# Kernel tuning notes

Measured on AMD Instinct MI355X. Metric: run time of the kernel, lower is better.

The kernel has to match this reference:

```python
import jax, jax.numpy as jnp
import numpy as np

# Production-scale dims: tokens T = B*S = 1024, d_model = 768, 8 experts, top-2 routing
B, S, D, E, K = 1, 1024, 768, 8, 2
H = 4 * D  # expert hidden dim


def setup_inputs() -> dict:
    key = jax.random.key(0)
    ks = jax.random.split(key, 6)
    s = jnp.float32(0.02)
    return {
        "x": jax.random.normal(ks[0], (B, S, D), jnp.float32),
        "Wr": jax.random.normal(ks[1], (E, D), jnp.float32) * s,      # router Linear (no bias), torch layout [out,in]
        "W1": jax.random.normal(ks[2], (E, H, D), jnp.float32) * s,   # per-expert first Linear
        "b1": jnp.zeros((E, H), jnp.float32),
        "W2": jax.random.normal(ks[3], (E, D, H), jnp.float32) * s,   # per-expert second Linear
        "b2": jnp.zeros((E, D), jnp.float32),
        "sW1": jax.random.normal(ks[4], (H, D), jnp.float32) * s,     # shared expert
        "sb1": jnp.zeros((H,), jnp.float32),
        "sW2": jax.random.normal(ks[5], (D, H), jnp.float32) * s,
        "sb2": jnp.zeros((D,), jnp.float32),
    }


def reference(x, Wr, W1, b1, W2, b2, sW1, sb1, sW2, sb2):
    Bx, Sx, Dx = x.shape
    xf = x.reshape(-1, Dx)                                   # [T, D]
    T = xf.shape[0]

    # Router: top-k logits, others masked to -inf, then softmax.
    # softmax over -inf-masked logits == softmax over the k kept logits scattered back.
    logits = xf @ Wr.T                                       # [T, E]
    topv, idx = jax.lax.top_k(logits, K)                     # [T, K]
    gate_k = jax.nn.softmax(topv, axis=-1)                   # [T, K]
    gates = jnp.zeros((T, logits.shape[-1]), x.dtype).at[
        jnp.arange(T)[:, None], idx
    ].add(gate_k)                                            # [T, E], zero for unrouted experts

    # Expert MLPs (dense over experts; gate is exactly zero for unrouted -> same math
    # as the original masked gather/scatter loop). Dropout is identity in eval mode.
    h = jax.nn.relu(jnp.einsum('td,ehd->teh', xf, W1) + b1)  # [T, E, H]
    y = jnp.einsum('teh,edh->ted', h, W2) + b2               # [T, E, D]
    moe = jnp.einsum('te,ted->td', gates, y)                 # [T, D]

    # Shared expert: original adds 0.1 * shared(x) once per expert that selected the
    # token; every token is selected by exactly K (distinct top-k) experts.
    sh = jax.nn.relu(xf @ sW1.T + sb1) @ sW2.T + sb2         # [T, D]
    out = moe + (0.1 * K) * sh
    return out.reshape(Bx, Sx, Dx)
```

## Files before the change

kernel.cpp:

```cpp
#include <hip/hip_runtime.h>

#define T_TOK 1024
#define Dm 768
#define Hm 3072
#define NE 8
#define NPACK 3072
#define MAXTILES 32

typedef __attribute__((ext_vector_type(8))) short short8;
typedef __attribute__((ext_vector_type(4))) float f32x4;

__device__ __forceinline__ unsigned f2bf(float f) {
  unsigned u = __builtin_bit_cast(unsigned, f);
  u += 0x7fffu + ((u >> 16) & 1u);
  return u >> 16;
}
__device__ __forceinline__ unsigned pk2bf(float a, float b) {
  return f2bf(a) | (f2bf(b) << 16);
}

__global__ __launch_bounds__(256) void router_kernel(
    const float* __restrict__ x, const float* __restrict__ Wr,
    int* __restrict__ counts, int* __restrict__ tlist, float* __restrict__ glist,
    int4* __restrict__ tok2row, float2* __restrict__ tok2g) {
  __shared__ float sWr[NE * Dm];
  for (int i = threadIdx.x; i < NE * Dm; i += 256) sWr[i] = Wr[i];
  __syncthreads();
  const int wave = threadIdx.x >> 6, lane = threadIdx.x & 63;
  const int t = blockIdx.x * 4 + wave;
  float acc[NE];
#pragma unroll
  for (int e = 0; e < NE; e++) acc[e] = 0.f;
  for (int d = lane; d < Dm; d += 64) {
    float xv = x[t * Dm + d];
#pragma unroll
    for (int e = 0; e < NE; e++) acc[e] += xv * sWr[e * Dm + d];
  }
#pragma unroll
  for (int e = 0; e < NE; e++) {
#pragma unroll
    for (int off = 32; off > 0; off >>= 1) acc[e] += __shfl_down(acc[e], off);
  }
  if (lane == 0) {
    int i0 = 0; float v0 = acc[0];
#pragma unroll
    for (int e = 1; e < NE; e++) if (acc[e] > v0) { v0 = acc[e]; i0 = e; }
    int i1 = -1; float v1 = -1e30f;
#pragma unroll
    for (int e = 0; e < NE; e++) if (e != i0 && acc[e] > v1) { v1 = acc[e]; i1 = e; }
    float g0 = 1.f / (1.f + expf(v1 - v0));
    float g1 = 1.f - g0;
    int p0 = atomicAdd(&counts[i0], 1);
    tlist[i0 * T_TOK + p0] = t; glist[i0 * T_TOK + p0] = g0;
    int p1 = atomicAdd(&counts[i1], 1);
    tlist[i1 * T_TOK + p1] = t; glist[i1 * T_TOK + p1] = g1;
    tok2row[t] = make_int4(i0, p0, i1, p1);
    tok2g[t] = float2{g0, g1};
  }
}

template <int MODE>
__global__ __launch_bounds__(512) void moe_gemm(
    const float* __restrict__ x,
    const float* __restrict__ W1, const float* __restrict__ b1,
    const float* __restrict__ sW1, const float* __restrict__ sb1,
    const float* __restrict__ W2, const float* __restrict__ b2,
    const float* __restrict__ sW2, const float* __restrict__ sb2,
    unsigned short* __restrict__ hbuf, float* __restrict__ ybuf, float* __restrict__ outp,
    const int* __restrict__ counts,
    const int* __restrict__ tlist, const float* __restrict__ glist) {
  int ti = blockIdx.y;
  int e = 0, m0 = 0, pbase = 0, Ne = 0;
  bool found = false;
  for (int ee = 0; ee <= NE; ee++) {
    int ne = (ee < NE) ? counts[ee] : T_TOK;
    int nt = (ne + 127) >> 7;
    if (!found) {
      if (ti < nt) { e = ee; Ne = ne; m0 = ti << 7; found = true; }
      else { ti -= nt; pbase += ne; }
    }
  }
  if (!found) return;
  const int n0 = blockIdx.x * 128;

  constexpr int Kfull = (MODE == 0) ? Dm : Hm;
  constexpr int KC    = (MODE == 0) ? Dm : (Hm / 2);
  constexpr int NK    = KC / 64;
  const int kbase = (MODE == 0) ? 0 : (blockIdx.z * KC);

  const float* Bw;
  const float* bias;
  if constexpr (MODE == 0) {
    Bw   = (e < NE) ? W1 + (size_t)e * Hm * Dm : sW1;
    bias = (e < NE) ? b1 + (size_t)e * Hm : sb1;
  } else {
    Bw   = (e < NE) ? W2 + (size_t)e * Dm * Hm : sW2;
    bias = (e < NE) ? b2 + (size_t)e * Dm : sb2;
  }

  __shared__ unsigned short sA[128][72];
  __shared__ unsigned short sB[128][72];

  const int tid = threadIdx.x;
  const int lane = tid & 63;
  const int wid = tid >> 6;
  const int wr = wid >> 2;
  const int wc = wid & 3;

  const float* aPtrF[4];
  const unsigned short* aPtrH[2];
  if constexpr (MODE == 0) {
#pragma unroll
    for (int c = 0; c < 4; c++) {
      int gi = m0 + c * 32 + (tid >> 4);
      int si = gi < Ne ? gi : Ne - 1;
      int tok = (e < NE) ? tlist[e * T_TOK + si] : si;
      aPtrF[c] = x + (size_t)tok * Dm + (tid & 15) * 4;
    }
  } else {
#pragma unroll
    for (int c = 0; c < 2; c++) {
      int prow = pbase + m0 + c * 64 + (tid >> 3);
      if (prow >= NPACK) prow = NPACK - 1;
      aPtrH[c] = hbuf + (size_t)prow * Hm + kbase + (tid & 7) * 8;
    }
  }
  const float* bPtrF[4];
#pragma unroll
  for (int c = 0; c < 4; c++) {
    int nrow = n0 + c * 32 + (tid >> 4);
    bPtrF[c] = Bw + (size_t)nrow * Kfull + kbase + (tid & 15) * 4;
  }

  f32x4 acc[4][2];
#pragma unroll
  for (int m = 0; m < 4; m++)
#pragma unroll
    for (int n = 0; n < 2; n++) acc[m][n] = (f32x4)0.0f;

  const int rF = tid >> 4;
  const int cF = (tid & 15) * 4;
  const int rH = tid >> 3;
  const int cH = (tid & 7) * 8;
  const int frow = lane & 15;
  const int fk = (lane >> 4) * 8;

  float4 aFA[4], bFA[4], aFB[4], bFB[4];
  uint4 aHA[2], aHB[2];

  auto stage_load_A = [&](int ko) {
    if constexpr (MODE == 0) {
#pragma unroll
      for (int c = 0; c < 4; c++) aFA[c] = *(const float4*)(aPtrF[c] + ko);
    } else {
#pragma unroll
      for (int c = 0; c < 2; c++) aHA[c] = *(const uint4*)(aPtrH[c] + ko);
    }
#pragma unroll
    for (int c = 0; c < 4; c++) bFA[c] = *(const float4*)(bPtrF[c] + ko);
  };
  auto stage_load_B = [&](int ko) {
    if constexpr (MODE == 0) {
#pragma unroll
      for (int c = 0; c < 4; c++) aFB[c] = *(const float4*)(aPtrF[c] + ko);
    } else {
#pragma unroll
      for (int c = 0; c < 2; c++) aHB[c] = *(const uint4*)(aPtrH[c] + ko);
    }
#pragma unroll
    for (int c = 0; c < 4; c++) bFB[c] = *(const float4*)(bPtrF[c] + ko);
  };
  auto stage_write_A = [&]() {
    if constexpr (MODE == 0) {
#pragma unroll
      for (int c = 0; c < 4; c++)
        *(uint2*)&sA[c * 32 + rF][cF] =
            make_uint2(pk2bf(aFA[c].x, aFA[c].y), pk2bf(aFA[c].z, aFA[c].w));
    } else {
#pragma unroll
      for (int c = 0; c < 2; c++) *(uint4*)&sA[c * 64 + rH][cH] = aHA[c];
    }
#pragma unroll
    for (int c = 0; c < 4; c++)
      *(uint2*)&sB[c * 32 + rF][cF] =
          make_uint2(pk2bf(bFA[c].x, bFA[c].y), pk2bf(bFA[c].z, bFA[c].w));
  };
  auto stage_write_B = [&]() {
    if constexpr (MODE == 0) {
#pragma unroll
      for (int c = 0; c < 4; c++)
        *(uint2*)&sA[c * 32 + rF][cF] =
            make_uint2(pk2bf(aFB[c].x, aFB[c].y), pk2bf(aFB[c].z, aFB[c].w));
    } else {
#pragma unroll
      for (int c = 0; c < 2; c++) *(uint4*)&sA[c * 64 + rH][cH] = aHB[c];
    }
#pragma unroll
    for (int c = 0; c < 4; c++)
      *(uint2*)&sB[c * 32 + rF][cF] =
          make_uint2(pk2bf(bFB[c].x, bFB[c].y), pk2bf(bFB[c].z, bFB[c].w));
  };
  auto do_mfma = [&]() {
#pragma unroll
    for (int kk = 0; kk < 2; kk++) {
      short8 af[4], bfr[2];
#pragma unroll
      for (int m = 0; m < 4; m++)
        af[m] = *(const short8*)&sA[wr * 64 + m * 16 + frow][kk * 32 + fk];
#pragma unroll
      for (int n = 0; n < 2; n++)
        bfr[n] = *(const short8*)&sB[wc * 32 + n * 16 + frow][kk * 32 + fk];
#pragma unroll
      for (int m = 0; m < 4; m++)
#pragma unroll
        for (int n = 0; n < 2; n++)
          acc[m][n] = __builtin_amdgcn_mfma_f32_16x16x32_bf16(af[m], bfr[n], acc[m][n], 0, 0, 0);
    }
  };

  stage_load_A(0);
  stage_load_B(64);

  for (int ks = 0; ks < NK; ks += 2) {
    stage_write_A();
    __syncthreads();
    if (ks + 2 < NK) stage_load_A((ks + 2) * 64);
    do_mfma();
    __syncthreads();
    stage_write_B();
    __syncthreads();
    if (ks + 3 < NK) stage_load_B((ks + 3) * 64);
    do_mfma();
    __syncthreads();
  }

#pragma unroll
  for (int m = 0; m < 4; m++) {
    int lr = wr * 64 + m * 16 + (lane >> 4) * 4;
#pragma unroll
    for (int n = 0; n < 2; n++) {
      int gc = n0 + wc * 32 + n * 16 + (lane & 15);
      float bv = bias[gc];
#pragma unroll
      for (int j = 0; j < 4; j++) {
        int gi = m0 + lr + j;
        if (gi >= Ne) continue;
        float v = acc[m][n][j];
        if constexpr (MODE == 0) {
          v += bv;
          v = v > 0.f ? v : 0.f;
          hbuf[(size_t)(pbase + gi) * Hm + gc] = (unsigned short)f2bf(v);
        } else if constexpr (MODE == 1) {
          ybuf[(size_t)blockIdx.z * NPACK * Dm + (size_t)(pbase + gi) * Dm + gc] = v;
        } else {
          int t; float g;
          if (e < NE) { t = tlist[e * T_TOK + gi]; g = glist[e * T_TOK + gi]; }
          else        { t = gi; g = 0.2f; }
          float add = g * (v + (kbase == 0 ? bv : 0.f));
          atomicAdd(&outp[(size_t)t * Dm + gc], add);
        }
      }
    }
  }
}

__global__ __launch_bounds__(256) void finalize_kernel(
    const float* __restrict__ ybuf, const int* __restrict__ counts,
    const int4* __restrict__ tok2row, const float2* __restrict__ tok2g,
    const float* __restrict__ b2, const float* __restrict__ sb2,
    float* __restrict__ out) {
  const int t = blockIdx.x;
  int bases[NE];
  int s = 0;
#pragma unroll
  for (int e = 0; e < NE; e++) { bases[e] = s; s += counts[e]; }
  const int4 rr = tok2row[t];
  const float2 gg = tok2g[t];
  const int r0 = bases[rr.x] + rr.y;
  const int r1 = bases[rr.z] + rr.w;
  const int rs = s + t;
  const float* y0 = ybuf;
  const float* y1 = ybuf + (size_t)NPACK * Dm;
  for (int d = threadIdx.x; d < Dm; d += 256) {
    float v0 = y0[(size_t)r0 * Dm + d] + y1[(size_t)r0 * Dm + d] + b2[rr.x * Dm + d];
    float v1 = y0[(size_t)r1 * Dm + d] + y1[(size_t)r1 * Dm + d] + b2[rr.z * Dm + d];
    float vs = y0[(size_t)rs * Dm + d] + y1[(size_t)rs * Dm + d] + sb2[d];
    out[(size_t)t * Dm + d] = gg.x * v0 + gg.y * v1 + 0.2f * vs;
  }
}

extern "C" void kernel_launch(void* const* d_in, const int* in_sizes, int n_in,
                              void* d_out, int out_size, void* d_ws, size_t ws_size,
                              hipStream_t stream) {
  const float* x   = (const float*)d_in[0];
  const float* Wr  = (const float*)d_in[1];
  const float* W1  = (const float*)d_in[2];
  const float* b1  = (const float*)d_in[3];
  const float* W2  = (const float*)d_in[4];
  const float* b2  = (const float*)d_in[5];
  const float* sW1 = (const float*)d_in[6];
  const float* sb1 = (const float*)d_in[7];
  const float* sW2 = (const float*)d_in[8];
  const float* sb2 = (const float*)d_in[9];
  float* out = (float*)d_out;

  char* ws = (char*)d_ws;
  int*    counts  = (int*)(ws + 0);
  int4*   tok2row = (int4*)(ws + 1024);
  float2* tok2g   = (float2*)(ws + 17408);
  int*    tlist   = (int*)(ws + 25600);
  float*  glist   = (float*)(ws + 58368);
  unsigned short* hbuf = (unsigned short*)(ws + 91136);
  float*  ybuf    = (float*)(ws + 18965504);
  const size_t NEED_YBUF = 37839872;

  (void)hipMemsetAsync(counts, 0, 128, stream);

  router_kernel<<<dim3(T_TOK / 4), 256, 0, stream>>>(x, Wr, counts, tlist, glist,
                                                     tok2row, tok2g);

  moe_gemm<0><<<dim3(Hm / 128, MAXTILES, 1), 512, 0, stream>>>(
      x, W1, b1, sW1, sb1, W2, b2, sW2, sb2, hbuf, ybuf, out, counts, tlist, glist);

  if (ws_size >= NEED_YBUF) {
    moe_gemm<1><<<dim3(Dm / 128, MAXTILES, 2), 512, 0, stream>>>(
        x, W1, b1, sW1, sb1, W2, b2, sW2, sb2, hbuf, ybuf, out, counts, tlist, glist);
    finalize_kernel<<<dim3(T_TOK), 256, 0, stream>>>(ybuf, counts, tok2row, tok2g,
                                                     b2, sb2, out);
  } else {
    (void)hipMemsetAsync(out, 0, (size_t)T_TOK * Dm * sizeof(float), stream);
    moe_gemm<2><<<dim3(Dm / 128, MAXTILES, 2), 512, 0, stream>>>(
        x, W1, b1, sW1, sb1, W2, b2, sW2, sb2, hbuf, ybuf, out, counts, tlist, glist);
  }
}
```

Measured before the change: 371.9 us.

## Drop split-K in second GEMM, use 128x96 tiles, bf16 ybuf, fused shared-expert output

The second expert GEMM no longer splits K across two z-slices. It uses a 128x96 tile with a 4x2 wave layout, so each block covers the full K=3072. Expert outputs go to a bf16 ybuf instead of two fp32 partial buffers, and the shared-expert rows write 0.2*(v+bias) straight into the output, which finalize then accumulates into. Launch grids are flattened to 1D with an N-fastest block ordering, meant to improve weight reuse in cache, and the glist and fallback atomic paths are removed. The aim is to cut ybuf traffic and the finalize reads, at the cost of fewer blocks in the second GEMM (longer K loop per block) and bf16 rounding of expert outputs.

After: 356.6 us. -4.1%, faster.

```diff
diff --git a/kernel.cpp b/kernel.cpp
--- a/kernel.cpp
+++ b/kernel.cpp
@@ -18,10 +18,14 @@
 __device__ __forceinline__ unsigned pk2bf(float a, float b) {
   return f2bf(a) | (f2bf(b) << 16);
 }
+__device__ __forceinline__ float bf2f(unsigned short s) {
+  unsigned u = ((unsigned)s) << 16;
+  return __builtin_bit_cast(float, u);
+}
 
 __global__ __launch_bounds__(256) void router_kernel(
     const float* __restrict__ x, const float* __restrict__ Wr,
-    int* __restrict__ counts, int* __restrict__ tlist, float* __restrict__ glist,
+    int* __restrict__ counts, int* __restrict__ tlist,
     int4* __restrict__ tok2row, float2* __restrict__ tok2g) {
   __shared__ float sWr[NE * Dm];
   for (int i = threadIdx.x; i < NE * Dm; i += 256) sWr[i] = Wr[i];
@@ -51,9 +55,9 @@
     float g0 = 1.f / (1.f + expf(v1 - v0));
     float g1 = 1.f - g0;
     int p0 = atomicAdd(&counts[i0], 1);
-    tlist[i0 * T_TOK + p0] = t; glist[i0 * T_TOK + p0] = g0;
+    tlist[i0 * T_TOK + p0] = t;
     int p1 = atomicAdd(&counts[i1], 1);
-    tlist[i1 * T_TOK + p1] = t; glist[i1 * T_TOK + p1] = g1;
+    tlist[i1 * T_TOK + p1] = t;
     tok2row[t] = make_int4(i0, p0, i1, p1);
     tok2g[t] = float2{g0, g1};
   }
@@ -64,12 +68,24 @@
     const float* __restrict__ x,
     const float* __restrict__ W1, const float* __restrict__ b1,
     const float* __restrict__ sW1, const float* __restrict__ sb1,
-    const float* __restrict__ W2, const float* __restrict__ b2,
-    const float* __restrict__ sW2, const float* __restrict__ sb2,
-    unsigned short* __restrict__ hbuf, float* __restrict__ ybuf, float* __restrict__ outp,
-    const int* __restrict__ counts,
-    const int* __restrict__ tlist, const float* __restrict__ glist) {
-  int ti = blockIdx.y;
+    const float* __restrict__ W2, const float* __restrict__ sW2,
+    const float* __restrict__ sb2,
+    unsigned short* __restrict__ hbuf, unsigned short* __restrict__ ybuf,
+    float* __restrict__ outp,
+    const int* __restrict__ counts, const int* __restrict__ tlist) {
+  constexpr int BN    = (MODE == 0) ? 128 : 96;
+  constexpr int Kfull = (MODE == 0) ? Dm : Hm;
+  constexpr int NK    = Kfull / 64;
+  constexpr int M_REP = (MODE == 0) ? 4 : 2;
+  constexpr int N_REP = (MODE == 0) ? 2 : 3;
+  constexpr int NBR   = BN / 32;
+
+  const int b = blockIdx.x;
+  int nIdx, ti;
+  if constexpr (MODE == 0) { nIdx = (b % 8) + 8 * ((b / 8) % 3); ti = b / 24; }
+  else                     { nIdx = b % 8;                        ti = b / 8;  }
+  const int n0 = nIdx * BN;
+
   int e = 0, m0 = 0, pbase = 0, Ne = 0;
   bool found = false;
   for (int ee = 0; ee <= NE; ee++) {
@@ -81,12 +97,6 @@
     }
   }
   if (!found) return;
-  const int n0 = blockIdx.x * 128;
-
-  constexpr int Kfull = (MODE == 0) ? Dm : Hm;
-  constexpr int KC    = (MODE == 0) ? Dm : (Hm / 2);
-  constexpr int NK    = KC / 64;
-  const int kbase = (MODE == 0) ? 0 : (blockIdx.z * KC);
 
   const float* Bw;
   const float* bias;
@@ -95,17 +105,18 @@
     bias = (e < NE) ? b1 + (size_t)e * Hm : sb1;
   } else {
     Bw   = (e < NE) ? W2 + (size_t)e * Dm * Hm : sW2;
-    bias = (e < NE) ? b2 + (size_t)e * Dm : sb2;
+    bias = sb2;
   }
 
   __shared__ unsigned short sA[128][72];
-  __shared__ unsigned short sB[128][72];
+  __shared__ unsigned short sB[BN][72];
 
   const int tid = threadIdx.x;
   const int lane = tid & 63;
   const int wid = tid >> 6;
-  const int wr = wid >> 2;
-  const int wc = wid & 3;
+  int rb, cb;
+  if constexpr (MODE == 0) { rb = (wid >> 2) * 64; cb = (wid & 3) * 32; }
+  else                     { rb = (wid >> 1) * 32; cb = (wid & 1) * 48; }
 
   const float* aPtrF[4];
   const unsigned short* aPtrH[2];
@@ -122,21 +133,21 @@
     for (int c = 0; c < 2; c++) {
       int prow = pbase + m0 + c * 64 + (tid >> 3);
       if (prow >= NPACK) prow = NPACK - 1;
-      aPtrH[c] = hbuf + (size_t)prow * Hm + kbase + (tid & 7) * 8;
-    }
-  }
-  const float* bPtrF[4];
-#pragma unroll
-  for (int c = 0; c < 4; c++) {
+      aPtrH[c] = hbuf + (size_t)prow * Hm + (tid & 7) * 8;
+    }
+  }
+  const float* bPtrF[NBR];
+#pragma unroll
+  for (int c = 0; c < NBR; c++) {
     int nrow = n0 + c * 32 + (tid >> 4);
-    bPtrF[c] = Bw + (size_t)nrow * Kfull + kbase + (tid & 15) * 4;
-  }
-
-  f32x4 acc[4][2];
-#pragma unroll
-  for (int m = 0; m < 4; m++)
-#pragma unroll
-    for (int n = 0; n < 2; n++) acc[m][n] = (f32x4)0.0f;
+    bPtrF[c] = Bw + (size_t)nrow * Kfull + (tid & 15) * 4;
+  }
+
+  f32x4 acc[M_REP][N_REP];
+#pragma unroll
+  for (int m = 0; m < M_REP; m++)
+#pragma unroll
+    for (int n = 0; n < N_REP; n++) acc[m][n] = (f32x4)0.0f;
 
   const int rF = tid >> 4;
   const int cF = (tid & 15) * 4;
@@ -145,7 +156,7 @@
   const int frow = lane & 15;
   const int fk = (lane >> 4) * 8;
 
-  float4 aFA[4], bFA[4], aFB[4], bFB[4];
+  float4 aFA[4], bFA[NBR], aFB[4], bFB[NBR];
   uint4 aHA[2], aHB[2];
 
   auto stage_load_A = [&](int ko) {
@@ -157,7 +168,7 @@
       for (int c = 0; c < 2; c++) aHA[c] = *(const uint4*)(aPtrH[c] + ko);
     }
 #pragma unroll
-    for (int c = 0; c < 4; c++) bFA[c] = *(const float4*)(bPtrF[c] + ko);
+    for (int c = 0; c < NBR; c++) bFA[c] = *(const float4*)(bPtrF[c] + ko);
   };
   auto stage_load_B = [&](int ko) {
     if constexpr (MODE == 0) {
@@ -168,7 +179,7 @@
       for (int c = 0; c < 2; c++) aHB[c] = *(const uint4*)(aPtrH[c] + ko);
     }
 #pragma unroll
-    for (int c = 0; c < 4; c++) bFB[c] = *(const float4*)(bPtrF[c] + ko);
+    for (int c = 0; c < NBR; c++) bFB[c] = *(const float4*)(bPtrF[c] + ko);
   };
   auto stage_write_A = [&]() {
     if constexpr (MODE == 0) {
@@ -181,7 +192,7 @@
       for (int c = 0; c < 2; c++) *(uint4*)&sA[c * 64 + rH][cH] = aHA[c];
     }
 #pragma unroll
-    for (int c = 0; c < 4; c++)
+    for (int c = 0; c < NBR; c++)
       *(uint2*)&sB[c * 32 + rF][cF] =
           make_uint2(pk2bf(bFA[c].x, bFA[c].y), pk2bf(bFA[c].z, bFA[c].w));
   };
@@ -196,24 +207,24 @@
       for (int c = 0; c < 2; c++) *(uint4*)&sA[c * 64 + rH][cH] = aHB[c];
     }
 #pragma unroll
-    for (int c = 0; c < 4; c++)
+    for (int c = 0; c < NBR; c++)
       *(uint2*)&sB[c * 32 + rF][cF] =
           make_uint2(pk2bf(bFB[c].x, bFB[c].y), pk2bf(bFB[c].z, bFB[c].w));
   };
   auto do_mfma = [&]() {
 #pragma unroll
     for (int kk = 0; kk < 2; kk++) {
-      short8 af[4], bfr[2];
-#pragma unroll
-      for (int m = 0; m < 4; m++)
-        af[m] = *(const short8*)&sA[wr * 64 + m * 16 + frow][kk * 32 + fk];
-#pragma unroll
-      for (int n = 0; n < 2; n++)
-        bfr[n] = *(const short8*)&sB[wc * 32 + n * 16 + frow][kk * 32 + fk];
-#pragma unroll
-      for (int m = 0; m < 4; m++)
-#pragma unroll
-        for (int n = 0; n < 2; n++)
+      short8 af[M_REP], bfr[N_REP];
+#pragma unroll
+      for (int m = 0; m < M_REP; m++)
+        af[m] = *(const short8*)&sA[rb + m * 16 + frow][kk * 32 + fk];
+#pragma unroll
+      for (int n = 0; n < N_REP; n++)
+        bfr[n] = *(const short8*)&sB[cb + n * 16 + frow][kk * 32 + fk];
+#pragma unroll
+      for (int m = 0; m < M_REP; m++)
+#pragma unroll
+        for (int n = 0; n < N_REP; n++)
           acc[m][n] = __builtin_amdgcn_mfma_f32_16x16x32_bf16(af[m], bfr[n], acc[m][n], 0, 0, 0);
     }
   };
@@ -235,29 +246,26 @@
   }
 
 #pragma unroll
-  for (int m = 0; m < 4; m++) {
-    int lr = wr * 64 + m * 16 + (lane >> 4) * 4;
-#pragma unroll
-    for (int n = 0; n < 2; n++) {
-      int gc = n0 + wc * 32 + n * 16 + (lane & 15);
-      float bv = bias[gc];
+  for (int m = 0; m < M_REP; m++) {
+    int lr = rb + m * 16 + (lane >> 4) * 4;
+#pragma unroll
+    for (int n = 0; n < N_REP; n++) {
+      int gc = n0 + cb + n * 16 + (lane & 15);
 #pragma unroll
       for (int j = 0; j < 4; j++) {
         int gi = m0 + lr + j;
         if (gi >= Ne) continue;
         float v = acc[m][n][j];
         if constexpr (MODE == 0) {
-          v += bv;
+          v += bias[gc];
           v = v > 0.f ? v : 0.f;
           hbuf[(size_t)(pbase + gi) * Hm + gc] = (unsigned short)f2bf(v);
-        } else if constexpr (MODE == 1) {
-          ybuf[(size_t)blockIdx.z * NPACK * Dm + (size_t)(pbase + gi) * Dm + gc] = v;
         } else {
-          int t; float g;
-          if (e < NE) { t = tlist[e * T_TOK + gi]; g = glist[e * T_TOK + gi]; }
-          else        { t = gi; g = 0.2f; }
-          float add = g * (v + (kbase == 0 ? bv : 0.f));
-          atomicAdd(&outp[(size_t)t * Dm + gc], add);
+          if (e < NE) {
+            ybuf[(size_t)(pbase + gi) * Dm + gc] = (unsigned short)f2bf(v);
+          } else {
+            outp[(size_t)gi * Dm + gc] = 0.2f * (v + bias[gc]);
+          }
         }
       }
     }
@@ -265,10 +273,9 @@
 }
 
 __global__ __launch_bounds__(256) void finalize_kernel(
-    const float* __restrict__ ybuf, const int* __restrict__ counts,
+    const unsigned short* __restrict__ ybuf, const int* __restrict__ counts,
     const int4* __restrict__ tok2row, const float2* __restrict__ tok2g,
-    const float* __restrict__ b2, const float* __restrict__ sb2,
-    float* __restrict__ out) {
+    const float* __restrict__ b2, float* __restrict__ out) {
   const int t = blockIdx.x;
   int bases[NE];
   int s = 0;
@@ -278,14 +285,10 @@
   const float2 gg = tok2g[t];
   const int r0 = bases[rr.x] + rr.y;
   const int r1 = bases[rr.z] + rr.w;
-  const int rs = s + t;
-  const float* y0 = ybuf;
-  const float* y1 = ybuf + (size_t)NPACK * Dm;
   for (int d = threadIdx.x; d < Dm; d += 256) {
-    float v0 = y0[(size_t)r0 * Dm + d] + y1[(size_t)r0 * Dm + d] + b2[rr.x * Dm + d];
-    float v1 = y0[(size_t)r1 * Dm + d] + y1[(size_t)r1 * Dm + d] + b2[rr.z * Dm + d];
-    float vs = y0[(size_t)rs * Dm + d] + y1[(size_t)rs * Dm + d] + sb2[d];
-    out[(size_t)t * Dm + d] = gg.x * v0 + gg.y * v1 + 0.2f * vs;
+    float v0 = bf2f(ybuf[(size_t)r0 * Dm + d]) + b2[rr.x * Dm + d];
+    float v1 = bf2f(ybuf[(size_t)r1 * Dm + d]) + b2[rr.z * Dm + d];
+    out[(size_t)t * Dm + d] += gg.x * v0 + gg.y * v1;
   }
 }
 
@@ -306,30 +309,20 @@
 
   char* ws = (char*)d_ws;
   int*    counts  = (int*)(ws + 0);
-  int4*   tok2row = (int4*)(ws + 1024);
-  float2* tok2g   = (float2*)(ws + 17408);
-  int*    tlist   = (int*)(ws + 25600);
-  float*  glist   = (float*)(ws + 58368);
-  unsigned short* hbuf = (unsigned short*)(ws + 91136);
-  float*  ybuf    = (float*)(ws + 18965504);
-  const size_t NEED_YBUF = 37839872;
+  int4*   tok2row = (int4*)(ws + 128);
+  float2* tok2g   = (float2*)(ws + 16512);
+  int*    tlist   = (int*)(ws + 24704);
+  unsigned short* hbuf = (unsigned short*)(ws + 57472);
+  unsigned short* ybuf = (unsigned short*)(ws + 18931840);
 
   (void)hipMemsetAsync(counts, 0, 128, stream);
 
-  router_kernel<<<dim3(T_TOK / 4), 256, 0, stream>>>(x, Wr, counts, tlist, glist,
-                                                     tok2row, tok2g);
-
-  moe_gemm<0><<<dim3(Hm / 128, MAXTILES, 1), 512, 0, stream>>>(
-      x, W1, b1, sW1, sb1, W2, b2, sW2, sb2, hbuf, ybuf, out, counts, tlist, glist);
-
-  if (ws_size >= NEED_YBUF) {
-    moe_gemm<1><<<dim3(Dm / 128, MAXTILES, 2), 512, 0, stream>>>(
-        x, W1, b1, sW1, sb1, W2, b2, sW2, sb2, hbuf, ybuf, out, counts, tlist, glist);
-    finalize_kernel<<<dim3(T_TOK), 256, 0, stream>>>(ybuf, counts, tok2row, tok2g,
-                                                     b2, sb2, out);
-  } else {
-    (void)hipMemsetAsync(out, 0, (size_t)T_TOK * Dm * sizeof(float), stream);
-    moe_gemm<2><<<dim3(Dm / 128, MAXTILES, 2), 512, 0, stream>>>(
-        x, W1, b1, sW1, sb1, W2, b2, sW2, sb2, hbuf, ybuf, out, counts, tlist, glist);
-  }
-}
+  router_kernel<<<dim3(T_TOK / 4), 256, 0, stream>>>(x, Wr, counts, tlist, tok2row, tok2g);
+
+  moe_gemm<0><<<dim3(24 * MAXTILES), 512, 0, stream>>>(
+      x, W1, b1, sW1, sb1, W2, sW2, sb2, hbuf, ybuf, out, counts, tlist);
+  moe_gemm<1><<<dim3(8 * MAXTILES), 512, 0, stream>>>(
+      x, W1, b1, sW1, sb1, W2, sW2, sb2, hbuf, ybuf, out, counts, tlist);
+
+  finalize_kernel<<<dim3(T_TOK), 256, 0, stream>>>(ybuf, counts, tok2row, tok2g, b2, out);
+}
```
